# Performance work log

Hardware: AMD Instinct MI355X
Metric: run time of the kernel (lower is better)

Reference implementation:

```python
import jax, jax.numpy as jnp
import numpy as np

ALPHA = 0.7
NUM_HEADS = 12
NUM_KV_HEADS = 6
HEAD_DIM = 64
ROPE_BASE = 10000.0


def ternary_quantize(w):
    thr = ALPHA * jnp.mean(jnp.abs(w))
    return jnp.sign(w) * (jnp.abs(w) >= thr).astype(w.dtype)


def bitlinear(x, w):
    # forward: F.linear(x, ternary(w)) * mean(|w|)
    scale = jnp.mean(jnp.abs(w))
    qw = ternary_quantize(w)
    return (x @ qw.T) * scale


def rope_tables(seq_len, dim, dtype):
    inv_freq = 1.0 / (ROPE_BASE ** (jnp.arange(0, dim, 2, dtype=jnp.float32) / dim))
    t = jnp.arange(seq_len, dtype=jnp.float32)
    freqs = jnp.outer(t, inv_freq)            # [S, dim/2]
    emb = jnp.concatenate([freqs, freqs], -1)  # [S, dim]
    return jnp.cos(emb).astype(dtype), jnp.sin(emb).astype(dtype)


def rotate_half(x):
    x1, x2 = jnp.split(x, 2, axis=-1)
    return jnp.concatenate([-x2, x1], axis=-1)


def setup_inputs() -> dict:
    key = jax.random.key(0)
    ks = jax.random.split(key, 5)
    B, S, H = 2, 2048, 768
    return {
        "hidden_states": jax.random.normal(ks[0], (B, S, H), jnp.float32),
        "Wq": jax.random.normal(ks[1], (768, 768), jnp.float32) * 0.02,
        "Wk": jax.random.normal(ks[2], (384, 768), jnp.float32) * 0.02,
        "Wv": jax.random.normal(ks[3], (384, 768), jnp.float32) * 0.02,
        "Wo": jax.random.normal(ks[4], (768, 768), jnp.float32) * 0.02,
    }


def reference(hidden_states, Wq, Wk, Wv, Wo):
    B, S, H = hidden_states.shape
    nh, nkv, hd = NUM_HEADS, NUM_KV_HEADS, HEAD_DIM
    groups = nh // nkv

    q = bitlinear(hidden_states, Wq).reshape(B, S, nh, hd).transpose(0, 2, 1, 3)
    k = bitlinear(hidden_states, Wk).reshape(B, S, nkv, hd).transpose(0, 2, 1, 3)
    v = bitlinear(hidden_states, Wv).reshape(B, S, nkv, hd).transpose(0, 2, 1, 3)

    cos, sin = rope_tables(S, hd, hidden_states.dtype)  # [S, hd]
    cos = cos[None, None]  # [1,1,S,hd]
    sin = sin[None, None]
    q = q * cos + rotate_half(q) * sin
    k = k * cos + rotate_half(k) * sin

    # GQA: expand kv heads to full head count
    k = jnp.repeat(k, groups, axis=1)  # [B, nh, S, hd]
    v = jnp.repeat(v, groups, axis=1)

    scale = 1.0 / jnp.sqrt(jnp.asarray(hd, hidden_states.dtype))
    scores = jnp.einsum("bhsd,bhtd->bhst", q, k) * scale
    attn = jax.nn.softmax(scores, axis=-1)
    out = jnp.einsum("bhst,bhtd->bhsd", attn, v)
    out = out.transpose(0, 2, 1, 3).reshape(B, S, H)
    return bitlinear(out, Wo)
```

## Files before the change

### kernel.cpp

```cpp
#include <hip/hip_runtime.h>
#include <cmath>

typedef unsigned short u16;
typedef unsigned int u32;
typedef __bf16 bf16x2 __attribute__((ext_vector_type(2)));
typedef __bf16 bf16x8 __attribute__((ext_vector_type(8)));
typedef float f32x2 __attribute__((ext_vector_type(2)));
typedef float f32x16 __attribute__((ext_vector_type(16)));

#define NQ (768*768)
#define NK (384*768)

__device__ __forceinline__ u16 f2bf(float f) {
  u32 u = __float_as_uint(f);
  u32 r = (u + 0x7FFFu + ((u >> 16) & 1u)) >> 16;
  return (u16)r;
}
__device__ __forceinline__ u32 packbf(float a, float b) {
#if __has_builtin(__builtin_amdgcn_cvt_pk_bf16_f32)
  bf16x2 v = __builtin_amdgcn_cvt_pk_bf16_f32(a, b);
  u32 r; __builtin_memcpy(&r, &v, 4); return r;
#else
  return (u32)f2bf(a) | ((u32)f2bf(b) << 16);
#endif
}
__device__ __forceinline__ float fexp2(float x) {
#if __has_builtin(__builtin_amdgcn_exp2f)
  return __builtin_amdgcn_exp2f(x);
#else
  return exp2f(x);
#endif
}
__device__ __forceinline__ bf16x8 ldfrag(const u16* p) { bf16x8 v; __builtin_memcpy(&v, p, 16); return v; }
__device__ __forceinline__ f32x16 mfma32_(bf16x8 a, bf16x8 b, f32x16 c) {
  return __builtin_amdgcn_mfma_f32_32x32x16_bf16(a, b, c, 0, 0, 0);
}
__device__ __forceinline__ void gload_lds16(const u16* g, u16* l) {
  __builtin_amdgcn_global_load_lds((const __attribute__((address_space(1))) void*)g,
                                   (__attribute__((address_space(3))) void*)l, 16, 0, 0);
}
__device__ __forceinline__ int xcd_swz768(int lin) { return (lin & 7) * 96 + (lin >> 3); }

__device__ __forceinline__ int fidx(int r, int k) {
  return (r >> 5) * 24576 + (k >> 4) * 512 + ((r & 31) + 32 * ((k >> 3) & 1)) * 8 + (k & 7);
}
__device__ __forceinline__ int kidx(int b6kvh, int s, int d) {
  return b6kvh * 131072 + (s >> 5) * 2048 + (d >> 4) * 512 +
         ((s & 31) + 32 * ((d >> 3) & 1)) * 8 + (d & 7);
}
__device__ __forceinline__ int qidx(int b, int s, int h, int d) {
  return ((b * 64 + (s >> 5)) * 12 + h) * 2048 + (d >> 4) * 512 +
         ((s & 31) + 32 * ((d >> 3) & 1)) * 8 + (d & 7);
}
__device__ __forceinline__ int vidx(int b6kvh, int d, int p) {
  return b6kvh * 131072 + (p >> 6) * 4096 + (d >> 5) * 2048 + ((p >> 4) & 3) * 512 +
         ((d & 31) + 32 * ((p >> 3) & 1)) * 8 + (p & 7);
}

__global__ __launch_bounds__(256) void abssum_kernel(const float* __restrict__ wq, const float* __restrict__ wk,
                                                     const float* __restrict__ wv, const float* __restrict__ wo,
                                                     float* __restrict__ sums) {
  int which = blockIdx.y;
  const float* w = (which == 0) ? wq : (which == 1) ? wk : (which == 2) ? wv : wo;
  int n4 = ((which == 0 || which == 3) ? NQ : NK) >> 2;
  const float4* w4 = (const float4*)w;
  float s = 0.f;
  for (int i = blockIdx.x * blockDim.x + threadIdx.x; i < n4; i += gridDim.x * blockDim.x) {
    float4 v = w4[i];
    s += fabsf(v.x) + fabsf(v.y) + fabsf(v.z) + fabsf(v.w);
  }
  for (int off = 32; off; off >>= 1) s += __shfl_down(s, off);
  __shared__ float ls[4];
  if ((threadIdx.x & 63) == 0) ls[threadIdx.x >> 6] = s;
  __syncthreads();
  if (threadIdx.x == 0) atomicAdd(&sums[which], ls[0] + ls[1] + ls[2] + ls[3]);
}

__global__ __launch_bounds__(256) void prep_kernel(const float* __restrict__ wq, const float* __restrict__ wk,
                                                   const float* __restrict__ wv, const float* __restrict__ wo,
                                                   const float* __restrict__ sums, const float* __restrict__ x,
                                                   u16* __restrict__ qw, u16* __restrict__ woq,
                                                   u16* __restrict__ xb, float2* __restrict__ rt) {
  int i = blockIdx.x * blockDim.x + threadIdx.x;
  if (i < 221184) {
    int n = i / 96, k8 = i - n * 96;
    const float* src; float th; u16* dst; int nd;
    if (n < 768)       { src = wq + n * 768;          th = 0.7f * sums[0] * (1.f / NQ); dst = qw;  nd = n; }
    else if (n < 1152) { src = wk + (n - 768) * 768;  th = 0.7f * sums[1] * (1.f / NK); dst = qw;  nd = n; }
    else if (n < 1536) { src = wv + (n - 1152) * 768; th = 0.7f * sums[2] * (1.f / NK); dst = qw;  nd = n; }
    else               { src = wo + (n - 1536) * 768; th = 0.7f * sums[3] * (1.f / NQ); dst = woq; nd = n - 1536; }
    const float4* sp = (const float4*)(src + k8 * 8);
    float4 v0 = sp[0], v1 = sp[1];
    float e[8] = {v0.x, v0.y, v0.z, v0.w, v1.x, v1.y, v1.z, v1.w};
    u16 o[8];
#pragma unroll
    for (int j = 0; j < 8; j++)
      o[j] = f2bf((fabsf(e[j]) >= th) ? ((e[j] > 0.f) ? 1.f : -1.f) : 0.f);
    __builtin_memcpy(dst + fidx(nd, k8 * 8), o, 16);
  } else if (i < 614400) {
    int j = i - 221184;
    int m = j / 96, k8 = j - m * 96;
    const float4* xp = (const float4*)(x + m * 768 + k8 * 8);
    float4 v0 = xp[0], v1 = xp[1];
    u16 o[8] = { f2bf(v0.x), f2bf(v0.y), f2bf(v0.z), f2bf(v0.w),
                 f2bf(v1.x), f2bf(v1.y), f2bf(v1.z), f2bf(v1.w) };
    __builtin_memcpy(xb + fidx(m, k8 * 8), o, 16);
  } else {
    int j = i - 614400;
    int s = j >> 5, c = j & 31;
    float f = exp2f((float)c * -0.41524101186092029f);
    float sn, cs; sincosf((float)s * f, &sn, &cs);
    rt[j] = make_float2(cs, sn);
  }
}

__global__ __launch_bounds__(256, 3) void gemm_qkv_kernel(const u16* __restrict__ xb, const u16* __restrict__ qw,
                                                          const float* __restrict__ sums,
                                                          const float2* __restrict__ rt,
                                                          u16* __restrict__ qb, u16* __restrict__ kb,
                                                          u16* __restrict__ vT) {
  __shared__ u16 sm[24 * 512];
  int v = xcd_swz768(blockIdx.x);
  int tm = v / 12, tn = v - tm * 12;
  int t = threadIdx.x, lane = t & 63, w = t >> 6, c = lane & 31, g2 = lane >> 5;
  int wm = w & 1, wn = w >> 1;
  int wn8 = wn * 8;

  f32x16 acc[2]; acc[0] = (f32x16)0.f; acc[1] = (f32x16)0.f;

  for (int s = 0; s < 12; ++s) {
#pragma unroll
    for (int i = 0; i < 6; i++) {
      int ch = w * 6 + i;
      const u16* src = (ch < 8)
        ? xb + (tm * 2 + (ch >> 2)) * 24576 + (s * 4 + (ch & 3)) * 512 + lane * 8
        : qw + (tn * 4 + (ch >> 2) - 2) * 24576 + (s * 4 + (ch & 3)) * 512 + lane * 8;
      gload_lds16(src, sm + ch * 512);
    }
    __syncthreads();
#pragma unroll
    for (int kc = 0; kc < 4; kc++) {
      bf16x8 a  = ldfrag(sm + (wm * 4 + kc) * 512 + lane * 8);
      bf16x8 b0 = ldfrag(sm + (8 + wn8 + kc) * 512 + lane * 8);
      bf16x8 b1 = ldfrag(sm + (12 + wn8 + kc) * 512 + lane * 8);
      acc[0] = mfma32_(a, b0, acc[0]);
      acc[1] = mfma32_(a, b1, acc[1]);
    }
    __syncthreads();
  }

  float sq = sums[0] * (1.f / NQ) * 0.180336880111120f;
  float sk = sums[1] * (1.f / NK);
  float sv = sums[2] * (1.f / NK);
  int mb = tm * 64 + wm * 32 + 4 * g2;
  if (tn < 9) {
    float sc = (tn < 6) ? sq : sk;
    int head = (tn < 6) ? (tn * 2 + wn) : ((tn - 6) * 2 + wn);
    const float2* rp = rt + c;
#pragma unroll
    for (int r = 0; r < 16; r++) {
      int m = mb + (r & 3) + 8 * (r >> 2);
      int bb = m >> 11, s = m & 2047;
      float2 cs2 = rp[s << 5];
      float x1 = acc[0][r] * sc, x2 = acc[1][r] * sc;
      u16 y1 = f2bf(x1 * cs2.x - x2 * cs2.y);
      u16 y2 = f2bf(x2 * cs2.x + x1 * cs2.y);
      if (tn < 6) {
        qb[qidx(bb, s, head, c)]      = y1;
        qb[qidx(bb, s, head, c + 32)] = y2;
      } else {
        kb[kidx(bb * 6 + head, s, c)]      = y1;
        kb[kidx(bb * 6 + head, s, c + 32)] = y2;
      }
    }
  } else {
    int kvh = (tn - 9) * 2 + wn;
#pragma unroll
    for (int nb = 0; nb < 2; nb++)
#pragma unroll
      for (int r = 0; r < 16; r++) {
        int m = mb + (r & 3) + 8 * (r >> 2);
        int bb = m >> 11, s = m & 2047;
        int sp = (s & ~12) | ((s & 4) << 1) | ((s & 8) >> 1);
        vT[vidx(bb * 6 + kvh, nb * 32 + c, sp)] = f2bf(acc[nb][r] * sv);
      }
  }
}

__device__ __forceinline__ void attn_step_pair(const bf16x8 (&kf)[4], const bf16x8 (&vf)[2][2],
                                               const bf16x8 (&qf0)[4], const bf16x8 (&qf1)[4],
                                               f32x16 (&O0)[2], f32x16 (&O1)[2],
                                               float& lsum0, float& lsum1) {
  f32x16 S = (f32x16)0.f;
  __builtin_amdgcn_s_setprio(1);
#pragma unroll
  for (int ks = 0; ks < 4; ks++) S = mfma32_(kf[ks], qf0[ks], S);
  __builtin_amdgcn_s_setprio(0);
#pragma unroll
  for (int r = 0; r < 16; r++) S[r] = fexp2(S[r]);
  {
    f32x2 a0 = {S[0], S[1]},  a1 = {S[2], S[3]},  a2 = {S[4], S[5]},  a3 = {S[6], S[7]};
    f32x2 a4 = {S[8], S[9]},  a5 = {S[10], S[11]}, a6 = {S[12], S[13]}, a7 = {S[14], S[15]};
    f32x2 b0 = a0 + a1, b1 = a2 + a3, b2 = a4 + a5, b3 = a6 + a7;
    f32x2 c0 = b0 + b1, c1 = b2 + b3;
    f32x2 d = c0 + c1;
    lsum0 += d.x + d.y;
  }
  u32 P[8];
#pragma unroll
  for (int j = 0; j < 8; j++) P[j] = packbf(S[2 * j], S[2 * j + 1]);
  bf16x8 PA0, PA1;
  __builtin_memcpy(&PA0, &P[0], 16);
  __builtin_memcpy(&PA1, &P[4], 16);
  f32x16 S1 = (f32x16)0.f;
  __builtin_amdgcn_s_setprio(1);
  O0[0] = mfma32_(PA0, vf[0][0], O0[0]);
  S1 = mfma32_(kf[0], qf1[0], S1);
  O0[1] = mfma32_(PA0, vf[1][0], O0[1]);
  S1 = mfma32_(kf[1], qf1[1], S1);
  O0[0] = mfma32_(PA1, vf[0][1], O0[0]);
  S1 = mfma32_(kf[2], qf1[2], S1);
  O0[1] = mfma32_(PA1, vf[1][1], O0[1]);
  S1 = mfma32_(kf[3], qf1[3], S1);
  __builtin_amdgcn_s_setprio(0);
#pragma unroll
  for (int r = 0; r < 16; r++) S1[r] = fexp2(S1[r]);
  {
    f32x2 a0 = {S1[0], S1[1]},  a1 = {S1[2], S1[3]},  a2 = {S1[4], S1[5]},  a3 = {S1[6], S1[7]};
    f32x2 a4 = {S1[8], S1[9]},  a5 = {S1[10], S1[11]}, a6 = {S1[12], S1[13]}, a7 = {S1[14], S1[15]};
    f32x2 b0 = a0 + a1, b1 = a2 + a3, b2 = a4 + a5, b3 = a6 + a7;
    f32x2 c0 = b0 + b1, c1 = b2 + b3;
    f32x2 d = c0 + c1;
    lsum1 += d.x + d.y;
  }
#pragma unroll
  for (int j = 0; j < 8; j++) P[j] = packbf(S1[2 * j], S1[2 * j + 1]);
  bf16x8 PB0, PB1;
  __builtin_memcpy(&PB0, &P[0], 16);
  __builtin_memcpy(&PB1, &P[4], 16);
  __builtin_amdgcn_s_setprio(1);
  O1[0] = mfma32_(PB0, vf[0][0], O1[0]);
  O1[1] = mfma32_(PB0, vf[1][0], O1[1]);
  O1[0] = mfma32_(PB1, vf[0][1], O1[0]);
  O1[1] = mfma32_(PB1, vf[1][1], O1[1]);
  __builtin_amdgcn_s_setprio(0);
}

__global__ __launch_bounds__(256, 3) void attn_kernel(const u16* __restrict__ qb, const u16* __restrict__ kb,
                                                      const u16* __restrict__ vT, u16* __restrict__ ab) {
  __shared__ float Obuf[4][32][66];
  __shared__ float Lbuf[4][32];
  int v = xcd_swz768(blockIdx.x);
  int bk = v >> 6, y = v & 63;
  int b = bk / 6, kvh = bk % 6;
  int qp = y & 31, h2 = y >> 5;
  int h = kvh * 2 + h2;
  int t = threadIdx.x, lane = t & 63, w = t >> 6, c = lane & 31, g2 = lane >> 5;

  const u16* q0 = qb + ((b * 64 + qp * 2) * 12 + h) * 2048 + lane * 8;
  const u16* q1 = q0 + 12 * 2048;
  bf16x8 qf0[4], qf1[4];
#pragma unroll
  for (int ks = 0; ks < 4; ks++) { qf0[ks] = ldfrag(q0 + ks * 512); qf1[ks] = ldfrag(q1 + ks * 512); }

  f32x16 fz = (f32x16)0.f;
  f32x16 O0[2] = {fz, fz}, O1[2] = {fz, fz};
  float lsum0 = 0.f, lsum1 = 0.f;

  const u16* Kb = kb + bk * 131072;
  const u16* Vb = vT + bk * 131072;

  for (int it = 0; it < 16; ++it) {
    int g = w * 16 + it;
    const u16* kt = Kb + g * 2048 + lane * 8;
    const u16* vt = Vb + (g >> 1) * 4096 + (g & 1) * 1024 + lane * 8;
    bf16x8 kf[4], vf[2][2];
#pragma unroll
    for (int ks = 0; ks < 4; ks++) kf[ks] = ldfrag(kt + ks * 512);
#pragma unroll
    for (int dn = 0; dn < 2; dn++)
#pragma unroll
      for (int ksv = 0; ksv < 2; ksv++)
        vf[dn][ksv] = ldfrag(vt + dn * 2048 + ksv * 512);
    attn_step_pair(kf, vf, qf0, qf1, O0, O1, lsum0, lsum1);
  }

  float lt0 = lsum0 + __shfl_xor(lsum0, 32);
  float lt1 = lsum1 + __shfl_xor(lsum1, 32);

#pragma unroll
  for (int qi = 0; qi < 2; qi++) {
    if (qi) __syncthreads();
    if (g2 == 0) Lbuf[w][c] = qi ? lt1 : lt0;
    const f32x16* Ow = qi ? O1 : O0;
#pragma unroll
    for (int dn = 0; dn < 2; dn++)
#pragma unroll
      for (int r = 0; r < 16; r++)
        Obuf[w][(r & 3) + 8 * (r >> 2) + 4 * g2][dn * 32 + c] = Ow[dn][r];
    __syncthreads();
    int qq = t >> 3, col8 = (t & 7) * 8;
    float l = Lbuf[0][qq] + Lbuf[1][qq] + Lbuf[2][qq] + Lbuf[3][qq];
    float inv = 1.f / l;
    u16 o[8];
#pragma unroll
    for (int j = 0; j < 8; j++)
      o[j] = f2bf((Obuf[0][qq][col8 + j] + Obuf[1][qq][col8 + j] +
                   Obuf[2][qq][col8 + j] + Obuf[3][qq][col8 + j]) * inv);
    int mg = b * 64 + qp * 2 + qi;
    u16* dst = ab + mg * 24576 + ((h * 64 + col8) >> 4) * 512 + ((col8 >> 3) & 1) * 256 + qq * 8;
    __builtin_memcpy(dst, o, 16);
  }
}

__global__ __launch_bounds__(256, 3) void gemm_out_kernel(const u16* __restrict__ ab, const u16* __restrict__ woq,
                                                          const float* __restrict__ sums, float* __restrict__ out) {
  int v = xcd_swz768(blockIdx.x);
  int tm = v / 12, tn = v - tm * 12;
  int t = threadIdx.x, lane = t & 63, w = t >> 6, c = lane & 31, g2 = lane >> 5;
  int wm = w & 1, wn = w >> 1;
  const u16* abase = ab + (tm * 2 + wm) * 24576 + lane * 8;
  const u16* bbase = woq + (tn * 2 + wn) * 24576 + lane * 8;
  f32x16 acc = (f32x16)0.f;
  bf16x8 aA[4], bA[4], aB[4], bB[4];
#pragma unroll
  for (int ks = 0; ks < 4; ks++) {
    aA[ks] = ldfrag(abase + ks * 512);
    bA[ks] = ldfrag(bbase + ks * 512);
  }
#pragma unroll
  for (int kk = 0; kk < 48; kk += 8) {
#pragma unroll
    for (int ks = 0; ks < 4; ks++) {
      aB[ks] = ldfrag(abase + (kk + 4 + ks) * 512);
      bB[ks] = ldfrag(bbase + (kk + 4 + ks) * 512);
    }
#pragma unroll
    for (int ks = 0; ks < 4; ks++) acc = mfma32_(aA[ks], bA[ks], acc);
    if (kk + 8 < 48) {
#pragma unroll
      for (int ks = 0; ks < 4; ks++) {
        aA[ks] = ldfrag(abase + (kk + 8 + ks) * 512);
        bA[ks] = ldfrag(bbase + (kk + 8 + ks) * 512);
      }
    }
#pragma unroll
    for (int ks = 0; ks < 4; ks++) acc = mfma32_(aB[ks], bB[ks], acc);
  }
  float so = sums[3] * (1.f / NQ);
  int mb = tm * 64 + wm * 32 + 4 * g2;
#pragma unroll
  for (int r = 0; r < 16; r++) {
    int m = mb + (r & 3) + 8 * (r >> 2);
    out[m * 768 + tn * 64 + wn * 32 + c] = acc[r] * so;
  }
}

extern "C" void kernel_launch(void* const* d_in, const int* in_sizes, int n_in,
                              void* d_out, int out_size, void* d_ws, size_t ws_size,
                              hipStream_t stream) {
  const float* x  = (const float*)d_in[0];
  const float* wq = (const float*)d_in[1];
  const float* wk = (const float*)d_in[2];
  const float* wv = (const float*)d_in[3];
  const float* wo = (const float*)d_in[4];
  float* out = (float*)d_out;
  char* ws = (char*)d_ws;

  float* sums = (float*)ws;
  u16* qw  = (u16*)(ws + 256);
  u16* woq = (u16*)(ws + 2359552);
  u16* xb  = (u16*)(ws + 3539200);
  u16* qb  = (u16*)(ws + 9830656);
  u16* kb  = (u16*)(ws + 16122112);
  u16* vT  = (u16*)(ws + 19267840);
  u16* ab  = (u16*)(ws + 22413568);
  float2* rt = (float2*)(ws + 28705024);

  hipMemsetAsync(sums, 0, 16, stream);
  dim3 blk(256);
  abssum_kernel<<<dim3(64, 4), blk, 0, stream>>>(wq, wk, wv, wo, sums);
  prep_kernel<<<dim3(2656), blk, 0, stream>>>(wq, wk, wv, wo, sums, x, qw, woq, xb, rt);
  gemm_qkv_kernel<<<dim3(768), blk, 0, stream>>>(xb, qw, sums, rt, qb, kb, vT);
  attn_kernel<<<dim3(768), blk, 0, stream>>>(qb, kb, vT, ab);
  gemm_out_kernel<<<dim3(768), blk, 0, stream>>>(ab, woq, sums, out);
}
```

Measured before the change: 145.9 us.

## Stage out-projection GEMM tiles through LDS and move RoPE table build into abssum

```diff
diff --git a/kernel.cpp b/kernel.cpp
--- a/kernel.cpp
+++ b/kernel.cpp
@@ -59,7 +59,7 @@
 
 __global__ __launch_bounds__(256) void abssum_kernel(const float* __restrict__ wq, const float* __restrict__ wk,
                                                      const float* __restrict__ wv, const float* __restrict__ wo,
-                                                     float* __restrict__ sums) {
+                                                     float* __restrict__ sums, float2* __restrict__ rt) {
   int which = blockIdx.y;
   const float* w = (which == 0) ? wq : (which == 1) ? wk : (which == 2) ? wv : wo;
   int n4 = ((which == 0 || which == 3) ? NQ : NK) >> 2;
@@ -74,13 +74,18 @@
   if ((threadIdx.x & 63) == 0) ls[threadIdx.x >> 6] = s;
   __syncthreads();
   if (threadIdx.x == 0) atomicAdd(&sums[which], ls[0] + ls[1] + ls[2] + ls[3]);
+  int gid = (blockIdx.y * 64 + blockIdx.x) * 256 + threadIdx.x;
+  int sr = gid >> 5, cc = gid & 31;
+  float f = exp2f((float)cc * -0.41524101186092029f);
+  float sn, cs; sincosf((float)sr * f, &sn, &cs);
+  rt[gid] = make_float2(cs, sn);
 }
 
 __global__ __launch_bounds__(256) void prep_kernel(const float* __restrict__ wq, const float* __restrict__ wk,
                                                    const float* __restrict__ wv, const float* __restrict__ wo,
                                                    const float* __restrict__ sums, const float* __restrict__ x,
                                                    u16* __restrict__ qw, u16* __restrict__ woq,
-                                                   u16* __restrict__ xb, float2* __restrict__ rt) {
+                                                   u16* __restrict__ xb) {
   int i = blockIdx.x * blockDim.x + threadIdx.x;
   if (i < 221184) {
     int n = i / 96, k8 = i - n * 96;
@@ -97,7 +102,7 @@
     for (int j = 0; j < 8; j++)
       o[j] = f2bf((fabsf(e[j]) >= th) ? ((e[j] > 0.f) ? 1.f : -1.f) : 0.f);
     __builtin_memcpy(dst + fidx(nd, k8 * 8), o, 16);
-  } else if (i < 614400) {
+  } else {
     int j = i - 221184;
     int m = j / 96, k8 = j - m * 96;
     const float4* xp = (const float4*)(x + m * 768 + k8 * 8);
@@ -105,12 +110,6 @@
     u16 o[8] = { f2bf(v0.x), f2bf(v0.y), f2bf(v0.z), f2bf(v0.w),
                  f2bf(v1.x), f2bf(v1.y), f2bf(v1.z), f2bf(v1.w) };
     __builtin_memcpy(xb + fidx(m, k8 * 8), o, 16);
-  } else {
-    int j = i - 614400;
-    int s = j >> 5, c = j & 31;
-    float f = exp2f((float)c * -0.41524101186092029f);
-    float sn, cs; sincosf((float)s * f, &sn, &cs);
-    rt[j] = make_float2(cs, sn);
   }
 }
 
@@ -315,38 +314,33 @@
 
 __global__ __launch_bounds__(256, 3) void gemm_out_kernel(const u16* __restrict__ ab, const u16* __restrict__ woq,
                                                           const float* __restrict__ sums, float* __restrict__ out) {
+  __shared__ u16 sm[32 * 512];
   int v = xcd_swz768(blockIdx.x);
   int tm = v / 12, tn = v - tm * 12;
   int t = threadIdx.x, lane = t & 63, w = t >> 6, c = lane & 31, g2 = lane >> 5;
   int wm = w & 1, wn = w >> 1;
-  const u16* abase = ab + (tm * 2 + wm) * 24576 + lane * 8;
-  const u16* bbase = woq + (tn * 2 + wn) * 24576 + lane * 8;
+
   f32x16 acc = (f32x16)0.f;
-  bf16x8 aA[4], bA[4], aB[4], bB[4];
-#pragma unroll
-  for (int ks = 0; ks < 4; ks++) {
-    aA[ks] = ldfrag(abase + ks * 512);
-    bA[ks] = ldfrag(bbase + ks * 512);
-  }
-#pragma unroll
-  for (int kk = 0; kk < 48; kk += 8) {
-#pragma unroll
-    for (int ks = 0; ks < 4; ks++) {
-      aB[ks] = ldfrag(abase + (kk + 4 + ks) * 512);
-      bB[ks] = ldfrag(bbase + (kk + 4 + ks) * 512);
-    }
-#pragma unroll
-    for (int ks = 0; ks < 4; ks++) acc = mfma32_(aA[ks], bA[ks], acc);
-    if (kk + 8 < 48) {
-#pragma unroll
-      for (int ks = 0; ks < 4; ks++) {
-        aA[ks] = ldfrag(abase + (kk + 8 + ks) * 512);
-        bA[ks] = ldfrag(bbase + (kk + 8 + ks) * 512);
-      }
-    }
-#pragma unroll
-    for (int ks = 0; ks < 4; ks++) acc = mfma32_(aB[ks], bB[ks], acc);
-  }
+
+  for (int s = 0; s < 6; ++s) {
+#pragma unroll
+    for (int i = 0; i < 8; i++) {
+      int ch = w * 8 + i;
+      const u16* src = (ch < 16)
+        ? ab + (tm * 2 + (ch >> 3)) * 24576 + (s * 8 + (ch & 7)) * 512 + lane * 8
+        : woq + (tn * 2 + (ch >> 3) - 2) * 24576 + (s * 8 + (ch & 7)) * 512 + lane * 8;
+      gload_lds16(src, sm + ch * 512);
+    }
+    __syncthreads();
+#pragma unroll
+    for (int kc = 0; kc < 8; kc++) {
+      bf16x8 a = ldfrag(sm + (wm * 8 + kc) * 512 + lane * 8);
+      bf16x8 b = ldfrag(sm + (16 + wn * 8 + kc) * 512 + lane * 8);
+      acc = mfma32_(a, b, acc);
+    }
+    __syncthreads();
+  }
+
   float so = sums[3] * (1.f / NQ);
   int mb = tm * 64 + wm * 32 + 4 * g2;
 #pragma unroll
@@ -379,8 +373,8 @@
 
   hipMemsetAsync(sums, 0, 16, stream);
   dim3 blk(256);
-  abssum_kernel<<<dim3(64, 4), blk, 0, stream>>>(wq, wk, wv, wo, sums);
-  prep_kernel<<<dim3(2656), blk, 0, stream>>>(wq, wk, wv, wo, sums, x, qw, woq, xb, rt);
+  abssum_kernel<<<dim3(64, 4), blk, 0, stream>>>(wq, wk, wv, wo, sums, rt);
+  prep_kernel<<<dim3(2400), blk, 0, stream>>>(wq, wk, wv, wo, sums, x, qw, woq, xb);
   gemm_qkv_kernel<<<dim3(768), blk, 0, stream>>>(xb, qw, sums, rt, qb, kb, vT);
   attn_kernel<<<dim3(768), blk, 0, stream>>>(qb, kb, vT, ab);
   gemm_out_kernel<<<dim3(768), blk, 0, stream>>>(ab, woq, sums, out);
```

After: 146.4 us (median of 2 runs). About the same (+0.3%).
